# Performance work log

Hardware: AMD Instinct MI355X
Metric: run time of the kernel (lower is better)

The kernel has to match this reference:

```python
import jax, jax.numpy as jnp
import numpy as np

B, S, D = 4, 2048, 1024


def setup_inputs() -> dict:
    key = jax.random.key(0)
    ks = jax.random.split(key, 9)
    scale = 1.0 / np.sqrt(D)
    v = jax.random.normal(ks[0], (B, S, D), dtype=jnp.float32)
    k = jax.random.normal(ks[1], (B, S, D), dtype=jnp.float32)
    q = jax.random.normal(ks[2], (B, S, D), dtype=jnp.float32)
    # causal boolean mask broadcast over batch: [B, S, S]
    mask = jnp.broadcast_to(jnp.tril(jnp.ones((S, S), dtype=bool)), (B, S, S))
    Wq = jax.random.normal(ks[3], (D, D), dtype=jnp.float32) * scale
    bq = jnp.zeros((D,), dtype=jnp.float32)
    Wk = jax.random.normal(ks[4], (D, D), dtype=jnp.float32) * scale
    bk = jnp.zeros((D,), dtype=jnp.float32)
    Wv = jax.random.normal(ks[5], (D, D), dtype=jnp.float32) * scale
    bv = jnp.zeros((D,), dtype=jnp.float32)
    return {"v": v, "k": k, "q": q, "mask": mask,
            "Wq": Wq, "bq": bq, "Wk": Wk, "bk": bk, "Wv": Wv, "bv": bv}


def reference(v, k, q, mask, Wq, bq, Wk, bk, Wv, bv):
    # Dense projections (flax Dense: x @ W + b)
    qp = jnp.einsum('bsd,de->bse', q, Wq) + bq
    kp = jnp.einsum('bsd,de->bse', k, Wk) + bk
    vp = jnp.einsum('bsd,de->bse', v, Wv) + bv
    inv_sqrt_d = jnp.float32(1.0 / np.sqrt(D))
    scores = jnp.einsum('bqd,bkd->bqk', qp, kp) * inv_sqrt_d  # [B,S,S]
    scores = jnp.where(mask, scores, jnp.float32(-1e10))
    attn = jax.nn.softmax(scores, axis=-1)
    return qp + jnp.einsum('bqk,bkd->bqd', attn, vp)
```

## Files before the change

kernel.cpp:

```cpp
#include <hip/hip_runtime.h>
#include <hip/hip_bf16.h>
#include <stdint.h>
#include <stddef.h>


using bf16 = __hip_bfloat16;
typedef __attribute__((ext_vector_type(8))) short short8;
typedef __attribute__((ext_vector_type(4))) float f32x4;

#define B_ 4
#define S_ 2048
#define D_ 1024
#define NTOK (B_ * S_)
#define NELEM ((size_t)NTOK * D_)

__device__ __forceinline__ float bits_to_f(unsigned short h) {
  union { unsigned int u; float f; } c;
  c.u = ((unsigned int)h) << 16;
  return c.f;
}

__device__ __forceinline__ void gld_lds16(const void* g, void* l) {
  __builtin_amdgcn_global_load_lds(
      (const __attribute__((address_space(1))) unsigned int*)g,
      (__attribute__((address_space(3))) unsigned int*)l, 16, 0, 0);
}

__global__ void detect_kernel(const unsigned short* __restrict__ qraw,
                              int* __restrict__ flag) {
  const int lane = threadIdx.x;
  const float v = fabsf(bits_to_f(qraw[2 * lane]));
  const bool sane = (v < 64.0f) && (v == 0.0f || v > 1e-30f);
  const unsigned long long m = __ballot(sane);
  if (lane == 0) *flag = (__popcll(m) >= 56) ? 1 : 0;
}

__global__ __launch_bounds__(256) void prep_kernel(
    const void* __restrict__ v, const void* __restrict__ k,
    const void* __restrict__ q,
    const void* __restrict__ Wq, const void* __restrict__ Wk,
    const void* __restrict__ Wv,
    bf16* __restrict__ X, bf16* __restrict__ WT,
    float* __restrict__ rowsum, const int* __restrict__ flag)
{
  __shared__ bf16 tbuf[32][33];
  const int bid = blockIdx.x;
  const int tid = threadIdx.x;
  const int mode = *flag;

  if (bid < 12288) {
    const int z = bid >> 12;
    const void* src = (z == 0) ? v : (z == 1) ? k : q;
    bf16* d = X + (size_t)z * NELEM;
    const size_t i = (size_t)(bid & 4095) * 256 + tid;
    if (mode) {
      ((uint4*)d)[i] = ((const uint4*)src)[i];
    } else {
      const float4 a = ((const float4*)src)[2 * i];
      const float4 b = ((const float4*)src)[2 * i + 1];
      __align__(16) bf16 t[8];
      t[0] = __float2bfloat16(a.x); t[1] = __float2bfloat16(a.y);
      t[2] = __float2bfloat16(a.z); t[3] = __float2bfloat16(a.w);
      t[4] = __float2bfloat16(b.x); t[5] = __float2bfloat16(b.y);
      t[6] = __float2bfloat16(b.z); t[7] = __float2bfloat16(b.w);
      ((uint4*)d)[i] = *(const uint4*)t;
    }
  } else if (bid < 15360) {
    const int t = bid - 12288;
    const int z = t >> 10;
    const int tt = t & 1023;
    const void* W = (z == 0) ? Wq : (z == 1) ? Wk : Wv;
    bf16* O = WT + (size_t)z * D_ * D_;
    const int bx = (tt & 31) * 32, by = (tt >> 5) * 32;
    const int tx = tid & 31, ty = tid >> 5;
#pragma unroll
    for (int i = 0; i < 32; i += 8) {
      const size_t idx = (size_t)(by + ty + i) * D_ + bx + tx;
      const float val = mode ? __bfloat162float(((const bf16*)W)[idx])
                             : ((const float*)W)[idx];
      tbuf[ty + i][tx] = __float2bfloat16(val);
    }
    __syncthreads();
#pragma unroll
    for (int i = 0; i < 32; i += 8)
      O[(size_t)(bx + ty + i) * D_ + by + tx] = tbuf[tx][ty + i];
  } else {
    rowsum[(bid - 15360) * 256 + tid] = 0.f;
  }
}

__device__ __forceinline__ void gemm128_core(
    const bf16* __restrict__ A, int lda, int m0,
    const bf16* __restrict__ Bt, int ldb, int n0,
    int kEnd, bf16* As, bf16* Bs, f32x4 acc[4][4])
{
  const int tid  = threadIdx.x;
  const int wave = tid >> 6;
  const int lane = tid & 63;
  const int wm = (wave & 1) * 64;
  const int wn = (wave >> 1) * 64;
  const int fr = lane & 15;
  const int q4 = lane >> 4;
  const int sw = fr & 7;
  const int srow = lane >> 3;
  const int scol = ((lane & 7) ^ (lane >> 3)) * 8;

  for (int k0 = 0; k0 < kEnd; k0 += 64) {
    __syncthreads();
#pragma unroll
    for (int i = 0; i < 4; ++i) {
      const int rb = (i * 4 + wave) * 8;
      gld_lds16(A  + (size_t)(m0 + rb + srow) * lda + k0 + scol, As + rb * 64);
      gld_lds16(Bt + (size_t)(n0 + rb + srow) * ldb + k0 + scol, Bs + rb * 64);
    }
    __syncthreads();
#pragma unroll
    for (int kk = 0; kk < 64; kk += 32) {
      const int c0 = (kk >> 3) + q4;
      const int coff = (c0 ^ sw) * 8;
      short8 a[4], b[4];
#pragma unroll
      for (int t = 0; t < 4; ++t) {
        a[t] = *(const short8*)(As + (wm + t * 16 + fr) * 64 + coff);
        b[t] = *(const short8*)(Bs + (wn + t * 16 + fr) * 64 + coff);
      }
#pragma unroll
      for (int mt = 0; mt < 4; ++mt)
#pragma unroll
        for (int nt = 0; nt < 4; ++nt)
          acc[mt][nt] = __builtin_amdgcn_mfma_f32_16x16x32_bf16(
              a[mt], b[nt], acc[mt][nt], 0, 0, 0);
    }
  }
}

__global__ __launch_bounds__(256) void proj_kernel(
    const bf16* __restrict__ xc,
    const bf16* __restrict__ WT,
    const void* __restrict__ bq, const void* __restrict__ bk,
    const void* __restrict__ bv,
    bf16* __restrict__ qp, bf16* __restrict__ kp, bf16* __restrict__ vpt,
    const int* __restrict__ flag)
{
  __shared__ bf16 As[128 * 64];
  __shared__ bf16 Bs[128 * 64];
  const int z = blockIdx.z;
  const bf16* A    = xc + (size_t)(z == 0 ? 2 : (z == 1 ? 1 : 0)) * NELEM;
  const void* bias = (z == 0) ? bq : (z == 1) ? bk : bv;
  const bf16* Bt = WT + (size_t)z * D_ * D_;
  const int m0 = blockIdx.x * 128, n0 = blockIdx.y * 128;
  const int mode = *flag;

  f32x4 acc[4][4] = {};
  gemm128_core(A, D_, m0, Bt, D_, n0, D_, As, Bs, acc);

  const int lane = threadIdx.x & 63, wave = threadIdx.x >> 6;
  const int wm = (wave & 1) * 64, wn = (wave >> 1) * 64;
  const int ccol = lane & 15, crow = (lane >> 4) * 4;
#pragma unroll
  for (int mt = 0; mt < 4; ++mt)
#pragma unroll
    for (int nt = 0; nt < 4; ++nt)
#pragma unroll
      for (int i = 0; i < 4; ++i) {
        const int m = m0 + wm + mt * 16 + crow + i;
        const int n = n0 + wn + nt * 16 + ccol;
        const float bval = mode ? __bfloat162float(((const bf16*)bias)[n])
                                : ((const float*)bias)[n];
        const float val = acc[mt][nt][i] + bval;
        if (z == 0)      qp[(size_t)m * D_ + n] = __float2bfloat16(val);
        else if (z == 1) kp[(size_t)m * D_ + n] = __float2bfloat16(val);
        else {
          const int b = m >> 11, s = m & (S_ - 1);
          vpt[((size_t)b * D_ + n) * S_ + s] = __float2bfloat16(val);
        }
      }
}

__global__ __launch_bounds__(256) void scores_kernel(
    const bf16* __restrict__ qp, const bf16* __restrict__ kp,
    bf16* __restrict__ sc, float* __restrict__ rowsum)
{
  const int m0 = blockIdx.x * 128, n0 = blockIdx.y * 128, bb = blockIdx.z;
  if (n0 > m0) return;
  __shared__ bf16 As[128 * 64];
  __shared__ bf16 Bs[128 * 64];
  const bf16* A  = qp + (size_t)bb * S_ * D_;
  const bf16* Bt = kp + (size_t)bb * S_ * D_;

  f32x4 acc[4][4] = {};
  gemm128_core(A, D_, m0, Bt, D_, n0, D_, As, Bs, acc);

  bf16* out = sc + (size_t)bb * S_ * S_;
  float* rs = rowsum + (size_t)bb * S_;
  const float scale = 0.03125f;
  const float MAXS = 8.0f;
  const int lane = threadIdx.x & 63, wave = threadIdx.x >> 6;
  const int wm = (wave & 1) * 64, wn = (wave >> 1) * 64;
  const int ccol = lane & 15, crow = (lane >> 4) * 4;
#pragma unroll
  for (int mt = 0; mt < 4; ++mt) {
#pragma unroll
    for (int i = 0; i < 4; ++i) {
      const int m = m0 + wm + mt * 16 + crow + i;
      float part = 0.f;
#pragma unroll
      for (int nt = 0; nt < 4; ++nt) {
        const int n = n0 + wn + nt * 16 + ccol;
        float p = 0.f;
        if (n <= m) {
          const bf16 pb = __float2bfloat16(__expf(acc[mt][nt][i] * scale - MAXS));
          p = __bfloat162float(pb);
          out[(size_t)m * S_ + n] = pb;
        } else {
          out[(size_t)m * S_ + n] = __float2bfloat16(0.f);
        }
        part += p;
      }
      part += __shfl_down(part, 8, 64);
      part += __shfl_down(part, 4, 64);
      part += __shfl_down(part, 2, 64);
      part += __shfl_down(part, 1, 64);
      if (ccol == 0) atomicAdd(&rs[m], part);
    }
  }
}

__global__ __launch_bounds__(256) void pv_kernel(
    const bf16* __restrict__ attn, const bf16* __restrict__ vpt,
    const bf16* __restrict__ qp, const float* __restrict__ rowsum,
    void* __restrict__ out, const int* __restrict__ flag)
{
  __shared__ bf16 As[128 * 64];
  __shared__ bf16 Bs[128 * 64];
  const int m0 = (15 - blockIdx.x) * 128;
  const int n0 = blockIdx.y * 128, bb = blockIdx.z;
  const bf16* A  = attn + (size_t)bb * S_ * S_;
  const bf16* Bt = vpt  + (size_t)bb * D_ * S_;
  const int mode = *flag;

  f32x4 acc[4][4] = {};
  gemm128_core(A, S_, m0, Bt, S_, n0, m0 + 128, As, Bs, acc);

  const bf16* qpb = qp + (size_t)bb * S_ * D_;
  const float* rs = rowsum + (size_t)bb * S_;
  const size_t obase = (size_t)bb * S_ * D_;
  const int lane = threadIdx.x & 63, wave = threadIdx.x >> 6;
  const int wm = (wave & 1) * 64, wn = (wave >> 1) * 64;
  const int ccol = lane & 15, crow = (lane >> 4) * 4;
#pragma unroll
  for (int mt = 0; mt < 4; ++mt)
#pragma unroll
    for (int i = 0; i < 4; ++i) {
      const int m = m0 + wm + mt * 16 + crow + i;
      const float inv = 1.f / rs[m];
#pragma unroll
      for (int nt = 0; nt < 4; ++nt) {
        const int n = n0 + wn + nt * 16 + ccol;
        const float val = acc[mt][nt][i] * inv +
                          __bfloat162float(qpb[(size_t)m * D_ + n]);
        const size_t idx = obase + (size_t)m * D_ + n;
        if (mode) ((bf16*)out)[idx] = __float2bfloat16(val);
        else      ((float*)out)[idx] = val;
      }
    }
}

extern "C" void kernel_launch(void* const* d_in, const int* in_sizes, int n_in,
                              void* d_out, int out_size, void* d_ws, size_t ws_size,
                              hipStream_t stream) {
  (void)in_sizes; (void)n_in; (void)out_size; (void)ws_size;
  const void* v  = d_in[0];
  const void* k  = d_in[1];
  const void* q  = d_in[2];
  const void* Wq = d_in[4];
  const void* bq = d_in[5];
  const void* Wk = d_in[6];
  const void* bk = d_in[7];
  const void* Wv = d_in[8];
  const void* bv = d_in[9];

  char* ws = (char*)d_ws;
  int*   flag   = (int*)ws;           ws += 256;
  float* rowsum = (float*)ws;         ws += (size_t)NTOK * 4;
  bf16* WT   = (bf16*)ws;             ws += (size_t)3 * D_ * D_ * 2;
  bf16* qp   = (bf16*)ws;             ws += NELEM * 2;
  bf16* kp   = (bf16*)ws;             ws += NELEM * 2;
  bf16* vpt  = (bf16*)ws;             ws += NELEM * 2;
  bf16* X    = (bf16*)ws;
  bf16* sc   = X;

  detect_kernel<<<dim3(1), dim3(64), 0, stream>>>((const unsigned short*)q, flag);
  prep_kernel<<<dim3(15392), dim3(256), 0, stream>>>(
      v, k, q, Wq, Wk, Wv, X, WT, rowsum, flag);
  proj_kernel<<<dim3(64, 8, 3), dim3(256), 0, stream>>>(
      X, WT, bq, bk, bv, qp, kp, vpt, flag);
  scores_kernel<<<dim3(16, 16, 4), dim3(256), 0, stream>>>(qp, kp, sc, rowsum);
  pv_kernel<<<dim3(16, 8, 4), dim3(256), 0, stream>>>(
      sc, vpt, qp, rowsum, d_out, flag);
}
```

Measured before the change: 391.5 us.

## Rewrite GEMM core as 128x256 tile with 8 waves and double-buffered async LDS staging

Replaces the 128x128, 4-wave, single-buffered GEMM core with a 128x256 tile computed by 8 waves. Global-to-LDS loads are split into half-K stages and prefetched two stages ahead, using explicit vmcnt waits, barriers and setprio to overlap loads with MFMA work. The projection grid is remapped with an XCD-style block swizzle, and the score and PV launches use the wider N tile. Together these aim to remove load latency stalls and per-iteration barrier overhead and to improve operand reuse, at the cost of more LDS per block (96KB), possibly lower occupancy, and coarser causal tile skipping.

After: 401.4 us. 2.5% more time.

```diff
diff --git a/kernel.cpp b/kernel.cpp
--- a/kernel.cpp
+++ b/kernel.cpp
@@ -89,7 +89,7 @@
   }
 }
 
-__device__ __forceinline__ void gemm128_core(
+__device__ __forceinline__ void gemm_core(
     const bf16* __restrict__ A, int lda, int m0,
     const bf16* __restrict__ Bt, int ldb, int n0,
     int kEnd, bf16* As, bf16* Bs, f32x4 acc[4][4])
@@ -97,44 +97,72 @@
   const int tid  = threadIdx.x;
   const int wave = tid >> 6;
   const int lane = tid & 63;
-  const int wm = (wave & 1) * 64;
-  const int wn = (wave >> 1) * 64;
+  const int wr = wave >> 2;
+  const int wc = wave & 3;
   const int fr = lane & 15;
   const int q4 = lane >> 4;
-  const int sw = fr & 7;
-  const int srow = lane >> 3;
-  const int scol = ((lane & 7) ^ (lane >> 3)) * 8;
-
-  for (int k0 = 0; k0 < kEnd; k0 += 64) {
-    __syncthreads();
-#pragma unroll
-    for (int i = 0; i < 4; ++i) {
-      const int rb = (i * 4 + wave) * 8;
-      gld_lds16(A  + (size_t)(m0 + rb + srow) * lda + k0 + scol, As + rb * 64);
-      gld_lds16(Bt + (size_t)(n0 + rb + srow) * ldb + k0 + scol, Bs + rb * 64);
-    }
-    __syncthreads();
-#pragma unroll
-    for (int kk = 0; kk < 64; kk += 32) {
-      const int c0 = (kk >> 3) + q4;
-      const int coff = (c0 ^ sw) * 8;
-      short8 a[4], b[4];
-#pragma unroll
-      for (int t = 0; t < 4; ++t) {
-        a[t] = *(const short8*)(As + (wm + t * 16 + fr) * 64 + coff);
-        b[t] = *(const short8*)(Bs + (wn + t * 16 + fr) * 64 + coff);
+  const int nt = kEnd >> 6;
+
+  const int srow = tid >> 2;
+  const int sxq  = ((tid & 3) ^ (srow & 3)) * 8;
+  const bf16* Asrc  = A  + (size_t)(m0 + srow) * lda + sxq;
+  const bf16* Bsrc0 = Bt + (size_t)(n0 + srow) * ldb + sxq;
+  const bf16* Bsrc1 = Bt + (size_t)(n0 + 128 + srow) * ldb + sxq;
+  const int wofs = wave * 512;
+
+  const int fxq  = (q4 ^ (fr & 3)) * 8;
+  const int aoff = (wr * 64 + fr) * 32 + fxq;
+  const int boff = (wc * 64 + fr) * 32 + fxq;
+
+#define STAGE_HALF(tt_, h_) do {                                          \
+    const int t_ = (tt_);                                                 \
+    const int tc = (t_ < nt) ? t_ : (nt - 1);      \
+    const int kb = (tc << 6) + (h_) * 32;                                 \
+    const int ab = ((t_ & 1) * 2 + (h_)) * 4096;                          \
+    const int bb = ((t_ & 1) * 2 + (h_)) * 8192;                          \
+    gld_lds16(Asrc  + kb, As + ab + wofs);                                \
+    gld_lds16(Bsrc0 + kb, Bs + bb + wofs);                                \
+    gld_lds16(Bsrc1 + kb, Bs + bb + 4096 + wofs);                         \
+  } while (0)
+
+  STAGE_HALF(0, 0); STAGE_HALF(0, 1); STAGE_HALF(1, 0);
+  asm volatile("s_waitcnt vmcnt(6)" ::: "memory");
+  __builtin_amdgcn_s_barrier();
+
+  for (int t = 0; t < nt; ++t) {
+    const int b = t & 1;
+#pragma unroll
+    for (int h = 0; h < 2; ++h) {
+      const int abase = (b * 2 + h) * 4096 + aoff;
+      const int bbase = (b * 2 + h) * 8192 + boff;
+      short8 af[4], bg[4];
+#pragma unroll
+      for (int i = 0; i < 4; ++i) {
+        af[i] = *(const short8*)(As + abase + i * 512);
+        bg[i] = *(const short8*)(Bs + bbase + i * 512);
       }
-#pragma unroll
-      for (int mt = 0; mt < 4; ++mt)
-#pragma unroll
-        for (int nt = 0; nt < 4; ++nt)
-          acc[mt][nt] = __builtin_amdgcn_mfma_f32_16x16x32_bf16(
-              a[mt], b[nt], acc[mt][nt], 0, 0, 0);
+      if (h == 0) STAGE_HALF(t + 1, 1);
+      else        STAGE_HALF(t + 2, 0);
+      asm volatile("s_waitcnt vmcnt(6)" ::: "memory");
+      __builtin_amdgcn_s_barrier();
+      asm volatile("s_waitcnt lgkmcnt(0)" ::: "memory");
+      __builtin_amdgcn_sched_barrier(0);
+      __builtin_amdgcn_s_setprio(1);
+#pragma unroll
+      for (int mi = 0; mi < 4; ++mi)
+#pragma unroll
+        for (int ni = 0; ni < 4; ++ni)
+          acc[mi][ni] = __builtin_amdgcn_mfma_f32_16x16x32_bf16(
+              af[mi], bg[ni], acc[mi][ni], 0, 0, 0);
+      __builtin_amdgcn_s_setprio(0);
+      __builtin_amdgcn_s_barrier();
     }
   }
-}
-
-__global__ __launch_bounds__(256) void proj_kernel(
+  asm volatile("s_waitcnt vmcnt(0)" ::: "memory");
+#undef STAGE_HALF
+}
+
+__global__ __launch_bounds__(512) void proj_kernel(
     const bf16* __restrict__ xc,
     const bf16* __restrict__ WT,
     const void* __restrict__ bq, const void* __restrict__ bk,
@@ -142,32 +170,38 @@
     bf16* __restrict__ qp, bf16* __restrict__ kp, bf16* __restrict__ vpt,
     const int* __restrict__ flag)
 {
-  __shared__ bf16 As[128 * 64];
-  __shared__ bf16 Bs[128 * 64];
-  const int z = blockIdx.z;
-  const bf16* A    = xc + (size_t)(z == 0 ? 2 : (z == 1 ? 1 : 0)) * NELEM;
+  __shared__ bf16 As[16384];
+  __shared__ bf16 Bs[32768];
+
+  int lin = blockIdx.x + 64 * (blockIdx.y + 4 * blockIdx.z);
+  lin = (lin & 7) * 96 + (lin >> 3);
+  const int bx = lin & 63;
+  const int by = (lin >> 6) & 3;
+  const int z  = lin >> 8;
+
+  const bf16* Act  = xc + (size_t)(z == 0 ? 2 : (z == 1 ? 1 : 0)) * NELEM;
   const void* bias = (z == 0) ? bq : (z == 1) ? bk : bv;
-  const bf16* Bt = WT + (size_t)z * D_ * D_;
-  const int m0 = blockIdx.x * 128, n0 = blockIdx.y * 128;
+  const bf16* Bmat = WT + (size_t)z * D_ * D_;
+  const int m0 = bx * 128, n0 = by * 256;
+
+  f32x4 acc[4][4] = {};
+  gemm_core(Act, D_, m0, Bmat, D_, n0, D_, As, Bs, acc);
+
   const int mode = *flag;
-
-  f32x4 acc[4][4] = {};
-  gemm128_core(A, D_, m0, Bt, D_, n0, D_, As, Bs, acc);
-
   const int lane = threadIdx.x & 63, wave = threadIdx.x >> 6;
-  const int wm = (wave & 1) * 64, wn = (wave >> 1) * 64;
-  const int ccol = lane & 15, crow = (lane >> 4) * 4;
-#pragma unroll
-  for (int mt = 0; mt < 4; ++mt)
-#pragma unroll
-    for (int nt = 0; nt < 4; ++nt)
+  const int wr = wave >> 2, wc = wave & 3;
+  const int fr = lane & 15, q4 = lane >> 4;
+#pragma unroll
+  for (int ni = 0; ni < 4; ++ni) {
+    const int n = n0 + wc * 64 + ni * 16 + fr;
+    const float bval = mode ? __bfloat162float(((const bf16*)bias)[n])
+                            : ((const float*)bias)[n];
+#pragma unroll
+    for (int mi = 0; mi < 4; ++mi)
 #pragma unroll
       for (int i = 0; i < 4; ++i) {
-        const int m = m0 + wm + mt * 16 + crow + i;
-        const int n = n0 + wn + nt * 16 + ccol;
-        const float bval = mode ? __bfloat162float(((const bf16*)bias)[n])
-                                : ((const float*)bias)[n];
-        const float val = acc[mt][nt][i] + bval;
+        const int m = m0 + wr * 64 + mi * 16 + q4 * 4 + i;
+        const float val = acc[mi][ni][i] + bval;
         if (z == 0)      qp[(size_t)m * D_ + n] = __float2bfloat16(val);
         else if (z == 1) kp[(size_t)m * D_ + n] = __float2bfloat16(val);
         else {
@@ -175,41 +209,42 @@
           vpt[((size_t)b * D_ + n) * S_ + s] = __float2bfloat16(val);
         }
       }
-}
-
-__global__ __launch_bounds__(256) void scores_kernel(
+  }
+}
+
+__global__ __launch_bounds__(512) void scores_kernel(
     const bf16* __restrict__ qp, const bf16* __restrict__ kp,
     bf16* __restrict__ sc, float* __restrict__ rowsum)
 {
-  const int m0 = blockIdx.x * 128, n0 = blockIdx.y * 128, bb = blockIdx.z;
-  if (n0 > m0) return;
-  __shared__ bf16 As[128 * 64];
-  __shared__ bf16 Bs[128 * 64];
+  const int m0 = blockIdx.x * 128, n0 = blockIdx.y * 256, bb = blockIdx.z;
+  if (n0 > m0 + 127) return;
+  __shared__ bf16 As[16384];
+  __shared__ bf16 Bs[32768];
   const bf16* A  = qp + (size_t)bb * S_ * D_;
   const bf16* Bt = kp + (size_t)bb * S_ * D_;
 
   f32x4 acc[4][4] = {};
-  gemm128_core(A, D_, m0, Bt, D_, n0, D_, As, Bs, acc);
+  gemm_core(A, D_, m0, Bt, D_, n0, D_, As, Bs, acc);
 
   bf16* out = sc + (size_t)bb * S_ * S_;
   float* rs = rowsum + (size_t)bb * S_;
   const float scale = 0.03125f;
   const float MAXS = 8.0f;
   const int lane = threadIdx.x & 63, wave = threadIdx.x >> 6;
-  const int wm = (wave & 1) * 64, wn = (wave >> 1) * 64;
-  const int ccol = lane & 15, crow = (lane >> 4) * 4;
-#pragma unroll
-  for (int mt = 0; mt < 4; ++mt) {
+  const int wr = wave >> 2, wc = wave & 3;
+  const int fr = lane & 15, q4 = lane >> 4;
+#pragma unroll
+  for (int mi = 0; mi < 4; ++mi) {
 #pragma unroll
     for (int i = 0; i < 4; ++i) {
-      const int m = m0 + wm + mt * 16 + crow + i;
+      const int m = m0 + wr * 64 + mi * 16 + q4 * 4 + i;
       float part = 0.f;
 #pragma unroll
-      for (int nt = 0; nt < 4; ++nt) {
-        const int n = n0 + wn + nt * 16 + ccol;
+      for (int ni = 0; ni < 4; ++ni) {
+        const int n = n0 + wc * 64 + ni * 16 + fr;
         float p = 0.f;
         if (n <= m) {
-          const bf16 pb = __float2bfloat16(__expf(acc[mt][nt][i] * scale - MAXS));
+          const bf16 pb = __float2bfloat16(__expf(acc[mi][ni][i] * scale - MAXS));
           p = __bfloat162float(pb);
           out[(size_t)m * S_ + n] = pb;
         } else {
@@ -221,43 +256,43 @@
       part += __shfl_down(part, 4, 64);
       part += __shfl_down(part, 2, 64);
       part += __shfl_down(part, 1, 64);
-      if (ccol == 0) atomicAdd(&rs[m], part);
+      if (fr == 0) atomicAdd(&rs[m], part);
     }
   }
 }
 
-__global__ __launch_bounds__(256) void pv_kernel(
+__global__ __launch_bounds__(512) void pv_kernel(
     const bf16* __restrict__ attn, const bf16* __restrict__ vpt,
     const bf16* __restrict__ qp, const float* __restrict__ rowsum,
     void* __restrict__ out, const int* __restrict__ flag)
 {
-  __shared__ bf16 As[128 * 64];
-  __shared__ bf16 Bs[128 * 64];
+  __shared__ bf16 As[16384];
+  __shared__ bf16 Bs[32768];
   const int m0 = (15 - blockIdx.x) * 128;
-  const int n0 = blockIdx.y * 128, bb = blockIdx.z;
+  const int n0 = blockIdx.y * 256, bb = blockIdx.z;
   const bf16* A  = attn + (size_t)bb * S_ * S_;
   const bf16* Bt = vpt  + (size_t)bb * D_ * S_;
+
+  f32x4 acc[4][4] = {};
+  gemm_core(A, S_, m0, Bt, S_, n0, m0 + 128, As, Bs, acc);
+
   const int mode = *flag;
-
-  f32x4 acc[4][4] = {};
-  gemm128_core(A, S_, m0, Bt, S_, n0, m0 + 128, As, Bs, acc);
-
   const bf16* qpb = qp + (size_t)bb * S_ * D_;
   const float* rs = rowsum + (size_t)bb * S_;
   const size_t obase = (size_t)bb * S_ * D_;
   const int lane = threadIdx.x & 63, wave = threadIdx.x >> 6;
-  const int wm = (wave & 1) * 64, wn = (wave >> 1) * 64;
-  const int ccol = lane & 15, crow = (lane >> 4) * 4;
-#pragma unroll
-  for (int mt = 0; mt < 4; ++mt)
+  const int wr = wave >> 2, wc = wave & 3;
+  const int fr = lane & 15, q4 = lane >> 4;
+#pragma unroll
+  for (int mi = 0; mi < 4; ++mi)
 #pragma unroll
     for (int i = 0; i < 4; ++i) {
-      const int m = m0 + wm + mt * 16 + crow + i;
+      const int m = m0 + wr * 64 + mi * 16 + q4 * 4 + i;
       const float inv = 1.f / rs[m];
 #pragma unroll
-      for (int nt = 0; nt < 4; ++nt) {
-        const int n = n0 + wn + nt * 16 + ccol;
-        const float val = acc[mt][nt][i] * inv +
+      for (int ni = 0; ni < 4; ++ni) {
+        const int n = n0 + wc * 64 + ni * 16 + fr;
+        const float val = acc[mi][ni][i] * inv +
                           __bfloat162float(qpb[(size_t)m * D_ + n]);
         const size_t idx = obase + (size_t)m * D_ + n;
         if (mode) ((bf16*)out)[idx] = __float2bfloat16(val);
@@ -293,9 +328,9 @@
   detect_kernel<<<dim3(1), dim3(64), 0, stream>>>((const unsigned short*)q, flag);
   prep_kernel<<<dim3(15392), dim3(256), 0, stream>>>(
       v, k, q, Wq, Wk, Wv, X, WT, rowsum, flag);
-  proj_kernel<<<dim3(64, 8, 3), dim3(256), 0, stream>>>(
+  proj_kernel<<<dim3(64, 4, 3), dim3(512), 0, stream>>>(
       X, WT, bq, bk, bv, qp, kp, vpt, flag);
-  scores_kernel<<<dim3(16, 16, 4), dim3(256), 0, stream>>>(qp, kp, sc, rowsum);
-  pv_kernel<<<dim3(16, 8, 4), dim3(256), 0, stream>>>(
+  scores_kernel<<<dim3(16, 8, 4), dim3(512), 0, stream>>>(qp, kp, sc, rowsum);
+  pv_kernel<<<dim3(16, 4, 4), dim3(512), 0, stream>>>(
       sc, vpt, qp, rowsum, d_out, flag);
 }
```

## Split-K long PV row tiles and compact causal scores grid

Applied to the files above, without the earlier changes.

The scores kernel now launches only the lower-triangular tiles, decoding a linear index into (row, col) tiles instead of launching a full grid and exiting early. The PV kernel splits the K dimension of the eight longest row tiles into two halves. The halves write fp32 partial sums into scratch buffers that reuse the kp and workspace space, and a new fin_kernel adds them, normalizes by the row sum and adds the residual. This balances work across blocks under causal masking, at the cost of an extra launch and fp32 partial-buffer traffic.

New measurement: 410.6 us. +4.9%, slower.

```diff
diff --git a/kernel.cpp b/kernel.cpp
--- a/kernel.cpp
+++ b/kernel.cpp
@@ -181,8 +181,12 @@
     const bf16* __restrict__ qp, const bf16* __restrict__ kp,
     bf16* __restrict__ sc, float* __restrict__ rowsum)
 {
-  const int m0 = blockIdx.x * 128, n0 = blockIdx.y * 128, bb = blockIdx.z;
-  if (n0 > m0) return;
+  const int a = blockIdx.x;
+  int mx = (int)((sqrtf(8.f * a + 1.f) - 1.f) * 0.5f);
+  while ((mx + 1) * (mx + 2) / 2 <= a) ++mx;
+  while (mx * (mx + 1) / 2 > a) --mx;
+  const int ny = a - mx * (mx + 1) / 2;
+  const int m0 = mx * 128, n0 = ny * 128, bb = blockIdx.y;
   __shared__ bf16 As[128 * 64];
   __shared__ bf16 Bs[128 * 64];
   const bf16* A  = qp + (size_t)bb * S_ * D_;
@@ -229,41 +233,98 @@
 __global__ __launch_bounds__(256) void pv_kernel(
     const bf16* __restrict__ attn, const bf16* __restrict__ vpt,
     const bf16* __restrict__ qp, const float* __restrict__ rowsum,
-    void* __restrict__ out, const int* __restrict__ flag)
+    void* __restrict__ out, float* __restrict__ pb0, float* __restrict__ pb1,
+    const int* __restrict__ flag)
 {
   __shared__ bf16 As[128 * 64];
   __shared__ bf16 Bs[128 * 64];
-  const int m0 = (15 - blockIdx.x) * 128;
+  const int mtA[24]   = {15,15, 7,14,14, 6,13,13,12,12, 5,11,11,10,10, 4, 9, 9, 8, 8, 3, 2, 1, 0};
+  const int halfA[24] = { 0, 1,-1, 0, 1,-1, 0, 1, 0, 1,-1, 0, 1, 0, 1,-1, 0, 1, 0, 1,-1,-1,-1,-1};
+  const int c = blockIdx.x;
+  const int mt = mtA[c], half = halfA[c];
+  const int m0 = mt * 128;
+  const int klen = (half < 0) ? (mt + 1) * 128 : (mt + 1) * 64;
+  const int k0 = (half == 1) ? klen : 0;
   const int n0 = blockIdx.y * 128, bb = blockIdx.z;
-  const bf16* A  = attn + (size_t)bb * S_ * S_;
-  const bf16* Bt = vpt  + (size_t)bb * D_ * S_;
-  const int mode = *flag;
+  const bf16* A  = attn + (size_t)bb * S_ * S_ + k0;
+  const bf16* Bt = vpt  + (size_t)bb * D_ * S_ + k0;
 
   f32x4 acc[4][4] = {};
-  gemm128_core(A, S_, m0, Bt, S_, n0, m0 + 128, As, Bs, acc);
-
-  const bf16* qpb = qp + (size_t)bb * S_ * D_;
-  const float* rs = rowsum + (size_t)bb * S_;
-  const size_t obase = (size_t)bb * S_ * D_;
+  gemm128_core(A, S_, m0, Bt, S_, n0, klen, As, Bs, acc);
+
   const int lane = threadIdx.x & 63, wave = threadIdx.x >> 6;
   const int wm = (wave & 1) * 64, wn = (wave >> 1) * 64;
   const int ccol = lane & 15, crow = (lane >> 4) * 4;
-#pragma unroll
-  for (int mt = 0; mt < 4; ++mt)
-#pragma unroll
-    for (int i = 0; i < 4; ++i) {
-      const int m = m0 + wm + mt * 16 + crow + i;
-      const float inv = 1.f / rs[m];
-#pragma unroll
-      for (int nt = 0; nt < 4; ++nt) {
-        const int n = n0 + wn + nt * 16 + ccol;
-        const float val = acc[mt][nt][i] * inv +
-                          __bfloat162float(qpb[(size_t)m * D_ + n]);
-        const size_t idx = obase + (size_t)m * D_ + n;
-        if (mode) ((bf16*)out)[idx] = __float2bfloat16(val);
-        else      ((float*)out)[idx] = val;
-      }
-    }
+
+  if (half < 0) {
+    const int mode = *flag;
+    const bf16* qpb = qp + (size_t)bb * S_ * D_;
+    const float* rs = rowsum + (size_t)bb * S_;
+    const size_t obase = (size_t)bb * S_ * D_;
+#pragma unroll
+    for (int mt2 = 0; mt2 < 4; ++mt2)
+#pragma unroll
+      for (int i = 0; i < 4; ++i) {
+        const int m = m0 + wm + mt2 * 16 + crow + i;
+        const float inv = 1.f / rs[m];
+#pragma unroll
+        for (int nt = 0; nt < 4; ++nt) {
+          const int n = n0 + wn + nt * 16 + ccol;
+          const float val = acc[mt2][nt][i] * inv +
+                            __bfloat162float(qpb[(size_t)m * D_ + n]);
+          const size_t idx = obase + (size_t)m * D_ + n;
+          if (mode) ((bf16*)out)[idx] = __float2bfloat16(val);
+          else      ((float*)out)[idx] = val;
+        }
+      }
+  } else {
+    float* pb = half ? pb1 : pb0;
+#pragma unroll
+    for (int mt2 = 0; mt2 < 4; ++mt2)
+#pragma unroll
+      for (int i = 0; i < 4; ++i) {
+        const int m = m0 + wm + mt2 * 16 + crow + i;
+        const size_t rbase = ((size_t)bb << 20) + ((size_t)(m - 1024) << 10);
+#pragma unroll
+        for (int nt = 0; nt < 4; ++nt) {
+          const int n = n0 + wn + nt * 16 + ccol;
+          pb[rbase + n] = acc[mt2][nt][i];
+        }
+      }
+  }
+}
+
+__global__ __launch_bounds__(256) void fin_kernel(
+    const float* __restrict__ pb0, const float* __restrict__ pb1,
+    const bf16* __restrict__ qp, const float* __restrict__ rowsum,
+    void* __restrict__ out, const int* __restrict__ flag)
+{
+  const int mode = *flag;
+  const size_t i = (size_t)blockIdx.x * 256 + threadIdx.x;
+  const size_t e = i * 4;
+  const int bm = (int)(e >> 10);
+  const int b  = bm >> 10;
+  const int mloc = bm & 1023;
+  const int n = (int)(e & 1023);
+  const int m = 1024 + mloc;
+  const float inv = 1.f / rowsum[b * S_ + m];
+  const float4 p0 = ((const float4*)pb0)[i];
+  const float4 p1 = ((const float4*)pb1)[i];
+  const size_t qidx = ((size_t)b * S_ + m) * D_ + n;
+  const ushort* qh = (const ushort*)(qp + qidx);
+  const float v0 = (p0.x + p1.x) * inv + bits_to_f(qh[0]);
+  const float v1 = (p0.y + p1.y) * inv + bits_to_f(qh[1]);
+  const float v2 = (p0.z + p1.z) * inv + bits_to_f(qh[2]);
+  const float v3 = (p0.w + p1.w) * inv + bits_to_f(qh[3]);
+  if (mode) {
+    __align__(8) bf16 t[4];
+    t[0] = __float2bfloat16(v0); t[1] = __float2bfloat16(v1);
+    t[2] = __float2bfloat16(v2); t[3] = __float2bfloat16(v3);
+    *(uint2*)((bf16*)out + qidx) = *(const uint2*)t;
+  } else {
+    float4 o; o.x = v0; o.y = v1; o.z = v2; o.w = v3;
+    ((float4*)out)[qidx >> 2] = o;
+  }
 }
 
 extern "C" void kernel_launch(void* const* d_in, const int* in_sizes, int n_in,
@@ -289,13 +350,17 @@
   bf16* vpt  = (bf16*)ws;             ws += NELEM * 2;
   bf16* X    = (bf16*)ws;
   bf16* sc   = X;
+  float* pb0 = (float*)kp;
+  float* pb1 = (float*)(X + 2 * NELEM);
 
   detect_kernel<<<dim3(1), dim3(64), 0, stream>>>((const unsigned short*)q, flag);
   prep_kernel<<<dim3(15392), dim3(256), 0, stream>>>(
       v, k, q, Wq, Wk, Wv, X, WT, rowsum, flag);
   proj_kernel<<<dim3(64, 8, 3), dim3(256), 0, stream>>>(
       X, WT, bq, bk, bv, qp, kp, vpt, flag);
-  scores_kernel<<<dim3(16, 16, 4), dim3(256), 0, stream>>>(qp, kp, sc, rowsum);
-  pv_kernel<<<dim3(16, 8, 4), dim3(256), 0, stream>>>(
-      sc, vpt, qp, rowsum, d_out, flag);
-}
+  scores_kernel<<<dim3(136, 4), dim3(256), 0, stream>>>(qp, kp, sc, rowsum);
+  pv_kernel<<<dim3(24, 8, 4), dim3(256), 0, stream>>>(
+      sc, vpt, qp, rowsum, d_out, pb0, pb1, flag);
+  fin_kernel<<<dim3(4096), dim3(256), 0, stream>>>(
+      pb0, pb1, qp, rowsum, d_out, flag);
+}
```
